# Kernel tuning notes

Measured on AMD Instinct MI355X. Metric: run time of the kernel, lower is better.

Reference implementation:

```python
import jax, jax.numpy as jnp
import numpy as np

H, D = 16, 64  # num_attention_heads, attention_head_size
BASE = 10000.0

def _rope(q, k, seq_len):
    # RotaryPositionalEmbedding: inv_freq over arange(0, D, 2); emb = cat(freqs, freqs)
    inv_freq = 1.0 / (BASE ** (jnp.arange(0, D, 2, dtype=jnp.float32) / D))  # [D/2]=32
    pos = jnp.arange(seq_len, dtype=jnp.float32)
    freqs = jnp.outer(pos, inv_freq)            # [S, 32]; equals cos_emb[..., :d]
    cos, sin = jnp.cos(freqs), jnp.sin(freqs)   # [S, 32]
    d = D // 2                                   # 32: only first half of head dim rotated
    half = d // 2                                # 16: internal rotate-half within rot part
    def rot(x):  # x: [B, H, S, D]
        xr, xp = x[..., :d], x[..., d:]
        swapped = jnp.concatenate([xr[..., half:], xr[..., :half]], axis=-1)
        xr2 = xr * cos - swapped * sin
        return jnp.concatenate([xr2, xp], axis=-1)
    return rot(q), rot(k)

def setup_inputs() -> dict:
    key = jax.random.key(0)
    ks = jax.random.split(key, 9)
    B, S, E = 2, 2048, 1024
    std = 0.02  # initializer_range
    inp = {"hidden_states": jax.random.normal(ks[0], (B, S, E), jnp.float32)}
    for i, n in enumerate(["q", "k", "v", "d"]):
        inp[f"W{n}"] = jax.random.normal(ks[1 + 2 * i], (E, E), jnp.float32) * std
        inp[f"b{n}"] = jnp.zeros((E,), jnp.float32)
    return inp

def reference(hidden_states, Wq, bq, Wk, bk, Wv, bv, Wd, bd):
    B, S, E = hidden_states.shape
    def heads(x):  # [B,S,E] -> [B,H,S,D]
        return x.reshape(B, S, H, D).transpose(0, 2, 1, 3)
    q = heads(hidden_states @ Wq + bq)
    k = heads(hidden_states @ Wk + bk)
    v = heads(hidden_states @ Wv + bv)
    q, k = _rope(q, k, S)
    scores = jnp.einsum("bhqd,bhkd->bhqk", q, k) / jnp.sqrt(jnp.float32(D))
    causal = jnp.tril(jnp.ones((S, S), dtype=bool))
    scores = jnp.where(causal, scores, -jnp.inf)
    probs = jax.nn.softmax(scores, axis=-1)
    ctx = jnp.einsum("bhqk,bhkd->bhqd", probs, v)
    ctx = ctx.transpose(0, 2, 1, 3).reshape(B, S, E)
    return ctx @ Wd + bd
```

## Files before the change

kernel.cpp:

```cpp
#include <hip/hip_runtime.h>
#include <stdint.h>

typedef __bf16 bf8 __attribute__((ext_vector_type(8)));
typedef float f4 __attribute__((ext_vector_type(4)));
typedef float f16v __attribute__((ext_vector_type(16)));
typedef unsigned short us8 __attribute__((ext_vector_type(8)));
typedef unsigned short us4 __attribute__((ext_vector_type(4)));

#define MFMA16(a, b, c) __builtin_amdgcn_mfma_f32_16x16x32_bf16(a, b, c, 0, 0, 0)
#define MFMA32(a, b, c) __builtin_amdgcn_mfma_f32_32x32x16_bf16(a, b, c, 0, 0, 0)

__device__ __forceinline__ unsigned short f2b(float f) {
  union { float f; unsigned u; } x; x.f = f;
  unsigned u = x.u;
  u += 0x7fffu + ((u >> 16) & 1u);
  return (unsigned short)(u >> 16);
}

__device__ __forceinline__ unsigned pk2(float a, float b) {
  union { float f; unsigned u; } ua, ub; ua.f = a; ub.f = b;
  return __builtin_amdgcn_perm(ub.u + 0x8000u, ua.u + 0x8000u, 0x07060302u);
}

__device__ __forceinline__ void plswap(unsigned &a, unsigned &b) {
  asm("v_permlane32_swap_b32 %0, %1" : "+v"(a), "+v"(b));
}

__device__ __forceinline__ void gload16(const void* g, void* l) {
  __builtin_amdgcn_global_load_lds(
      (const __attribute__((address_space(1))) void*)g,
      (__attribute__((address_space(3))) void*)l, 16, 0, 0);
}

__global__ __launch_bounds__(256) void prep_kernel(
    const float* __restrict__ W0, const float* __restrict__ W1,
    const float* __restrict__ W2, const float* __restrict__ W3,
    unsigned short* __restrict__ T0, unsigned short* __restrict__ T1,
    unsigned short* __restrict__ T2, unsigned short* __restrict__ T3,
    const float* __restrict__ hid, unsigned short* __restrict__ hb) {
  if (blockIdx.z == 4) {
    int bi = blockIdx.x + 32 * blockIdx.y;
#pragma unroll
    for (int k = 0; k < 4; ++k) {
      int i = bi * 1024 + k * 256 + threadIdx.x;
      float4 v = ((const float4*)hid)[i];
      us4 r = { f2b(v.x), f2b(v.y), f2b(v.z), f2b(v.w) };
      *(us4*)(hb + (size_t)i * 4) = r;
    }
    return;
  }
  const float* W; unsigned short* Wt;
  if (blockIdx.z == 0)      { W = W0; Wt = T0; }
  else if (blockIdx.z == 1) { W = W1; Wt = T1; }
  else if (blockIdx.z == 2) { W = W2; Wt = T2; }
  else                      { W = W3; Wt = T3; }
  __shared__ float tile[32][33];
  int tx = threadIdx.x & 31, ty = threadIdx.x >> 5;
  int kb = blockIdx.x * 32, nb = blockIdx.y * 32;
#pragma unroll
  for (int j = 0; j < 32; j += 8)
    tile[ty + j][tx] = W[(size_t)(kb + ty + j) * 1024 + nb + tx];
  __syncthreads();
#pragma unroll
  for (int j = 0; j < 32; j += 8)
    Wt[(size_t)(nb + ty + j) * 1024 + kb + tx] = f2b(tile[tx][ty + j]);
}

__global__ __launch_bounds__(256) void gemm_qkv_kernel(
    const unsigned short* __restrict__ X,
    const unsigned short* __restrict__ Wqt, const unsigned short* __restrict__ Wkt,
    const unsigned short* __restrict__ Wvt,
    const float* __restrict__ bq, const float* __restrict__ bk,
    const float* __restrict__ bv,
    unsigned short* __restrict__ Qo, unsigned short* __restrict__ Ko,
    unsigned short* __restrict__ Vo) {
  const unsigned short* Wt; const float* bias; unsigned short* out;
  if (blockIdx.z == 0)      { Wt = Wqt; bias = bq; out = Qo; }
  else if (blockIdx.z == 1) { Wt = Wkt; bias = bk; out = Ko; }
  else                      { Wt = Wvt; bias = bv; out = Vo; }

  __shared__ unsigned short As[128 * 32];
  __shared__ unsigned short Bs[128 * 32];
  const int t = threadIdx.x;
  const int wave = t >> 6, lane = t & 63, quad = lane >> 4, l16 = lane & 15;
  const int wm = (wave >> 1) * 64, wn = (wave & 1) * 64;
  const int m0 = blockIdx.y * 128, n0 = blockIdx.x * 128;

  f4 acc[4][4];
#pragma unroll
  for (int mi = 0; mi < 4; ++mi)
#pragma unroll
    for (int ni = 0; ni < 4; ++ni) acc[mi][ni] = (f4)0.0f;

  for (int k0 = 0; k0 < 1024; k0 += 32) {
    __syncthreads();
#pragma unroll
    for (int it = 0; it < 2; ++it) {
      int chunk = it * 256 + wave * 64 + lane;
      int row = chunk >> 2, c = chunk & 3;
      gload16(&X[(size_t)(m0 + row) * 1024 + k0 + c * 8],
              &As[(size_t)(it * 256 + wave * 64) * 8]);
      gload16(&Wt[(size_t)(n0 + row) * 1024 + k0 + c * 8],
              &Bs[(size_t)(it * 256 + wave * 64) * 8]);
    }
    __syncthreads();
    bf8 a[4], b[4];
#pragma unroll
    for (int mi = 0; mi < 4; ++mi)
      a[mi] = *(const bf8*)&As[(wm + mi * 16 + l16) * 32 + quad * 8];
#pragma unroll
    for (int ni = 0; ni < 4; ++ni)
      b[ni] = *(const bf8*)&Bs[(wn + ni * 16 + l16) * 32 + quad * 8];
#pragma unroll
    for (int mi = 0; mi < 4; ++mi)
#pragma unroll
      for (int ni = 0; ni < 4; ++ni)
        acc[mi][ni] = MFMA16(a[mi], b[ni], acc[mi][ni]);
  }

  float biasv[4];
#pragma unroll
  for (int ni = 0; ni < 4; ++ni) biasv[ni] = bias[n0 + wn + ni * 16 + l16];

  if (blockIdx.z < 2) {
    const float kr = 13.287712379549449f / 32.0f;
    const float f0 = exp2f(-(float)l16 * kr);
    const float f1 = exp2f(-(float)(l16 + 16) * kr);
    const float qs = (blockIdx.z == 0) ? 0.18033688011112042f : 1.0f;
#pragma unroll
    for (int mi = 0; mi < 4; ++mi) {
#pragma unroll
      for (int r = 0; r < 4; ++r) {
        int m = m0 + wm + mi * 16 + quad * 4 + r;
        float s = (float)(m & 2047);
        float s0, c0, s1, c1;
        __sincosf(s * f0, &s0, &c0);
        __sincosf(s * f1, &s1, &c1);
        float v0 = acc[mi][0][r] + biasv[0];
        float v1 = acc[mi][1][r] + biasv[1];
        acc[mi][0][r] = (v0 * c0 - v1 * s0) * qs;
        acc[mi][1][r] = (v1 * c1 - v0 * s1) * qs;
        acc[mi][2][r] = (acc[mi][2][r] + biasv[2]) * qs;
        acc[mi][3][r] = (acc[mi][3][r] + biasv[3]) * qs;
      }
    }
#pragma unroll
    for (int ni = 0; ni < 4; ++ni) {
      int n = n0 + wn + ni * 16 + l16;
      int h = n >> 6, d = n & 63;
#pragma unroll
      for (int mi = 0; mi < 4; ++mi) {
#pragma unroll
        for (int r = 0; r < 4; ++r) {
          int m = m0 + wm + mi * 16 + quad * 4 + r;
          int b_ = m >> 11, s = m & 2047;
          out[(size_t)(((b_ << 4) | h) * 2048 + s) * 64 + d] = f2b(acc[mi][ni][r]);
        }
      }
    }
  } else {
#pragma unroll
    for (int ni = 0; ni < 4; ++ni) {
      int n = n0 + wn + ni * 16 + l16;
      int h = n >> 6, d = n & 63;
#pragma unroll
      for (int mi = 0; mi < 4; ++mi) {
        int m = m0 + wm + mi * 16 + quad * 4;
        int b_ = m >> 11, s = m & 2047;
        us4 w = { f2b(acc[mi][ni][0] + biasv[ni]), f2b(acc[mi][ni][1] + biasv[ni]),
                  f2b(acc[mi][ni][2] + biasv[ni]), f2b(acc[mi][ni][3] + biasv[ni]) };
        *(us4*)&out[((size_t)(((b_ << 4) | h) * 64 + d)) * 2048 + s] = w;
      }
    }
  }
}

__global__ __launch_bounds__(256) void flash_attn_kernel(
    const unsigned short* __restrict__ Q, const unsigned short* __restrict__ K,
    const unsigned short* __restrict__ Vt, unsigned short* __restrict__ ctx) {
  __shared__ __align__(16) float osh[2][64][36];
  __shared__ float lsh[2][64];
  const int t = threadIdx.x;
  const int lane = t & 63;
  const int wave = t >> 6, l32 = lane & 31, hl = lane >> 5;
  const int sub = wave >> 1;
  const int kh  = wave & 1;

  const int id = blockIdx.x;
  const int bh = id & 31;
  const int j = id >> 5;
  const int qt = (j & 16) ? (31 - (j & 15)) : (j & 15);
  const int b = bh >> 4, h = bh & 15;

  const unsigned short* Qh = Q + (size_t)bh * 2048 * 64;
  const unsigned short* Kh = K + (size_t)bh * 2048 * 64;
  const unsigned short* Vh = Vt + (size_t)bh * 64 * 2048;

  const int wrow0 = qt * 64 + sub * 32;
  const int q = wrow0 + l32;

  bf8 qb[4];
#pragma unroll
  for (int c = 0; c < 4; ++c)
    qb[c] = *(const bf8*)&Qh[(size_t)q * 64 + c * 16 + hl * 8];

  f16v o0 = (f16v)0.0f, o1 = (f16v)0.0f;
  float sum = 0.0f;

  bf8 kfA[2][4], kfB[2][4], vf[2][4];
  const int nk = qt + 1;
  const int kb = kh ? (nk >> 1) : 0;
  const int ke = kh ? nk : (nk >> 1);

  auto loadK = [&](bf8 (&kf)[2][4], int k0) {
#pragma unroll
    for (int mt = 0; mt < 2; ++mt)
#pragma unroll
      for (int c = 0; c < 4; ++c)
        kf[mt][c] = *(const bf8*)&Kh[(size_t)(k0 + mt * 32 + l32) * 64 + c * 16 + hl * 8];
  };

  auto step = [&](int kt, bf8 (&kf)[2][4]) {
    const int k0 = kt * 64;
#pragma unroll
    for (int dt = 0; dt < 2; ++dt)
#pragma unroll
      for (int c = 0; c < 4; ++c)
        vf[dt][c] = *(const bf8*)&Vh[(size_t)(dt * 32 + l32) * 2048 + k0 + c * 16 + hl * 8];

    f16v s0 = (f16v)0.0f, s1 = (f16v)0.0f;
#pragma unroll
    for (int c = 0; c < 4; ++c) {
      s0 = MFMA32(kf[0][c], qb[c], s0);
      s1 = MFMA32(kf[1][c], qb[c], s1);
    }
    if (kt == nk - 1) {
#pragma unroll
      for (int gg = 0; gg < 4; ++gg)
#pragma unroll
        for (int i = 0; i < 4; ++i) {
          int kk = k0 + gg * 8 + hl * 4 + i;
          if (kk > q) s0[gg * 4 + i] = -3e38f;
          if (kk + 32 > q) s1[gg * 4 + i] = -3e38f;
        }
    }
    uint2 pd2[8];
#pragma unroll
    for (int gg = 0; gg < 4; ++gg) {
      float p0 = exp2f(s0[gg * 4 + 0]), p1 = exp2f(s0[gg * 4 + 1]);
      float p2 = exp2f(s0[gg * 4 + 2]), p3 = exp2f(s0[gg * 4 + 3]);
      sum += (p0 + p1) + (p2 + p3);
      pd2[gg].x = pk2(p0, p1); pd2[gg].y = pk2(p2, p3);
      float r0 = exp2f(s1[gg * 4 + 0]), r1 = exp2f(s1[gg * 4 + 1]);
      float r2 = exp2f(s1[gg * 4 + 2]), r3 = exp2f(s1[gg * 4 + 3]);
      sum += (r0 + r1) + (r2 + r3);
      pd2[4 + gg].x = pk2(r0, r1); pd2[4 + gg].y = pk2(r2, r3);
    }
    uint4 fr[4];
#pragma unroll
    for (int c = 0; c < 4; ++c) {
      unsigned ax = pd2[2 * c].x, bx = pd2[2 * c + 1].x;
      unsigned ay = pd2[2 * c].y, by = pd2[2 * c + 1].y;
      plswap(ax, bx);
      plswap(ay, by);
      fr[c].x = ax; fr[c].y = ay; fr[c].z = bx; fr[c].w = by;
    }
#pragma unroll
    for (int c = 0; c < 4; ++c) {
      union { uint4 u; bf8 v; } pv; pv.u = fr[c];
      o0 = MFMA32(vf[0][c], pv.v, o0);
      o1 = MFMA32(vf[1][c], pv.v, o1);
    }
  };

  if (kb < ke) {
    loadK(kfA, kb * 64);
    int kt = kb;
    while (true) {
      if (kt + 1 < ke) loadK(kfB, (kt + 1) * 64);
      step(kt, kfA);
      ++kt; if (kt >= ke) break;
      if (kt + 1 < ke) loadK(kfA, (kt + 1) * 64);
      step(kt, kfB);
      ++kt; if (kt >= ke) break;
    }
  }

  float lpart = sum + __shfl_xor(sum, 32);

  if (kh == 0) {
#pragma unroll
    for (int gg = 0; gg < 4; ++gg) {
      f4 w0 = { o0[gg * 4 + 0], o0[gg * 4 + 1], o0[gg * 4 + 2], o0[gg * 4 + 3] };
      *(f4*)&osh[sub][lane][gg * 4] = w0;
      f4 w1 = { o1[gg * 4 + 0], o1[gg * 4 + 1], o1[gg * 4 + 2], o1[gg * 4 + 3] };
      *(f4*)&osh[sub][lane][16 + gg * 4] = w1;
    }
    lsh[sub][lane] = lpart;
  }
  __syncthreads();
  if (kh == 1) {
    float inv = 1.0f / (lpart + lsh[sub][lane]);
#pragma unroll
    for (int gg = 0; gg < 4; ++gg) {
      int d0 = gg * 8 + hl * 4;
      f4 a0 = *(f4*)&osh[sub][lane][gg * 4];
      f4 a1 = *(f4*)&osh[sub][lane][16 + gg * 4];
      us4 w0 = { f2b((o0[gg * 4 + 0] + a0[0]) * inv), f2b((o0[gg * 4 + 1] + a0[1]) * inv),
                 f2b((o0[gg * 4 + 2] + a0[2]) * inv), f2b((o0[gg * 4 + 3] + a0[3]) * inv) };
      *(us4*)&ctx[((size_t)(b * 2048 + q)) * 1024 + h * 64 + d0] = w0;
      us4 w1 = { f2b((o1[gg * 4 + 0] + a1[0]) * inv), f2b((o1[gg * 4 + 1] + a1[1]) * inv),
                 f2b((o1[gg * 4 + 2] + a1[2]) * inv), f2b((o1[gg * 4 + 3] + a1[3]) * inv) };
      *(us4*)&ctx[((size_t)(b * 2048 + q)) * 1024 + h * 64 + 32 + d0] = w1;
    }
  }
}

__global__ __launch_bounds__(256) void gemm_out_kernel(
    const unsigned short* __restrict__ A,
    const unsigned short* __restrict__ Wt,
    const float* __restrict__ bias, float* __restrict__ out) {
  __shared__ unsigned short As[64 * 32];
  __shared__ unsigned short Bs[128 * 32];
  const int t = threadIdx.x;
  const int wave = t >> 6, lane = t & 63, quad = lane >> 4, l16 = lane & 15;
  const int wm = (wave & 1) * 32, wn = (wave >> 1) * 64;
  const int m0 = blockIdx.y * 64, n0 = blockIdx.x * 128;

  f4 acc[2][4];
#pragma unroll
  for (int mi = 0; mi < 2; ++mi)
#pragma unroll
    for (int ni = 0; ni < 4; ++ni) acc[mi][ni] = (f4)0.0f;

  for (int k0 = 0; k0 < 1024; k0 += 32) {
    __syncthreads();
    {
      int chunk = wave * 64 + lane;
      int row = chunk >> 2, c = chunk & 3;
      gload16(&A[(size_t)(m0 + row) * 1024 + k0 + c * 8],
              &As[(size_t)(wave * 64) * 8]);
#pragma unroll
      for (int it = 0; it < 2; ++it) {
        int ch = it * 256 + wave * 64 + lane;
        int rw = ch >> 2, cc = ch & 3;
        gload16(&Wt[(size_t)(n0 + rw) * 1024 + k0 + cc * 8],
                &Bs[(size_t)(it * 256 + wave * 64) * 8]);
      }
    }
    __syncthreads();
    bf8 a[2], b[4];
#pragma unroll
    for (int mi = 0; mi < 2; ++mi)
      a[mi] = *(const bf8*)&As[(wm + mi * 16 + l16) * 32 + quad * 8];
#pragma unroll
    for (int ni = 0; ni < 4; ++ni)
      b[ni] = *(const bf8*)&Bs[(wn + ni * 16 + l16) * 32 + quad * 8];
#pragma unroll
    for (int mi = 0; mi < 2; ++mi)
#pragma unroll
      for (int ni = 0; ni < 4; ++ni)
        acc[mi][ni] = MFMA16(a[mi], b[ni], acc[mi][ni]);
  }
#pragma unroll
  for (int ni = 0; ni < 4; ++ni) {
    int n = n0 + wn + ni * 16 + l16;
    float bv_ = bias[n];
#pragma unroll
    for (int mi = 0; mi < 2; ++mi) {
#pragma unroll
      for (int r = 0; r < 4; ++r) {
        int m = m0 + wm + mi * 16 + quad * 4 + r;
        out[(size_t)m * 1024 + n] = acc[mi][ni][r] + bv_;
      }
    }
  }
}

extern "C" void kernel_launch(void* const* d_in, const int* in_sizes, int n_in,
                              void* d_out, int out_size, void* d_ws, size_t ws_size,
                              hipStream_t stream) {
  const float* hidden = (const float*)d_in[0];
  const float* Wq = (const float*)d_in[1];
  const float* bq = (const float*)d_in[2];
  const float* Wk = (const float*)d_in[3];
  const float* bk = (const float*)d_in[4];
  const float* Wv = (const float*)d_in[5];
  const float* bv = (const float*)d_in[6];
  const float* Wd = (const float*)d_in[7];
  const float* bd = (const float*)d_in[8];
  float* out = (float*)d_out;

  char* ws = (char*)d_ws;
  unsigned short* Xb  = (unsigned short*)(ws);
  unsigned short* Wqt = (unsigned short*)(ws + ( 8ull << 20));
  unsigned short* Wkt = (unsigned short*)(ws + (10ull << 20));
  unsigned short* Wvt = (unsigned short*)(ws + (12ull << 20));
  unsigned short* Wdt = (unsigned short*)(ws + (14ull << 20));
  unsigned short* Qb  = (unsigned short*)(ws + (16ull << 20));
  unsigned short* Kb  = (unsigned short*)(ws + (24ull << 20));
  unsigned short* Vb  = (unsigned short*)(ws + (32ull << 20));
  unsigned short* Cb  = (unsigned short*)(ws + (40ull << 20));

  prep_kernel<<<dim3(32, 32, 5), 256, 0, stream>>>(
      Wq, Wk, Wv, Wd, Wqt, Wkt, Wvt, Wdt, hidden, Xb);
  gemm_qkv_kernel<<<dim3(8, 32, 3), 256, 0, stream>>>(
      Xb, Wqt, Wkt, Wvt, bq, bk, bv, Qb, Kb, Vb);
  flash_attn_kernel<<<1024, 256, 0, stream>>>(Qb, Kb, Vb, Cb);
  gemm_out_kernel<<<dim3(8, 64), 256, 0, stream>>>(Cb, Wdt, bd, out);
}
```

Before: 227.3 us.

## Store K and V in MFMA-fragment-tiled layout so attention loads are contiguous

The QKV projection epilogue now writes K and transposed V into a pre-swizzled layout that matches each lane's MFMA operand fragment for a 64-key tile. The flash attention kernel then loads each fragment as a fully contiguous per-lane 16-byte read (lane*8 offset) instead of strided row accesses. This is meant to improve coalescing and cut address arithmetic in the inner attention loop. The cost is scattered 2-byte stores for K in the projection epilogue, and the new layout couples the two kernels tightly.

```diff
diff --git a/kernel.cpp b/kernel.cpp
--- a/kernel.cpp
+++ b/kernel.cpp
@@ -144,32 +144,56 @@
         acc[mi][3][r] = (acc[mi][3][r] + biasv[3]) * qs;
       }
     }
+    if (blockIdx.z == 0) {
+#pragma unroll
+      for (int ni = 0; ni < 4; ++ni) {
+        int n = n0 + wn + ni * 16 + l16;
+        int h = n >> 6, d = n & 63;
+#pragma unroll
+        for (int mi = 0; mi < 4; ++mi) {
+#pragma unroll
+          for (int r = 0; r < 4; ++r) {
+            int m = m0 + wm + mi * 16 + quad * 4 + r;
+            int b_ = m >> 11, s = m & 2047;
+            out[(size_t)(((b_ << 4) | h) * 2048 + s) * 64 + d] = f2b(acc[mi][ni][r]);
+          }
+        }
+      }
+    } else {
+#pragma unroll
+      for (int ni = 0; ni < 4; ++ni) {
+        int n = n0 + wn + ni * 16 + l16;
+        int h = n >> 6, d = n & 63;
+        int cpart = (d >> 4) * 512 + ((d >> 3) & 1) * 256 + (d & 7);
+#pragma unroll
+        for (int mi = 0; mi < 4; ++mi) {
+#pragma unroll
+          for (int r = 0; r < 4; ++r) {
+            int m = m0 + wm + mi * 16 + quad * 4 + r;
+            int b_ = m >> 11, s = m & 2047;
+            size_t off = (size_t)((b_ << 4) | h) * 131072
+                       + (size_t)(s >> 5) * 2048 + (s & 31) * 8 + cpart;
+            out[off] = f2b(acc[mi][ni][r]);
+          }
+        }
+      }
+    }
+  } else {
 #pragma unroll
     for (int ni = 0; ni < 4; ++ni) {
       int n = n0 + wn + ni * 16 + l16;
       int h = n >> 6, d = n & 63;
-#pragma unroll
-      for (int mi = 0; mi < 4; ++mi) {
-#pragma unroll
-        for (int r = 0; r < 4; ++r) {
-          int m = m0 + wm + mi * 16 + quad * 4 + r;
-          int b_ = m >> 11, s = m & 2047;
-          out[(size_t)(((b_ << 4) | h) * 2048 + s) * 64 + d] = f2b(acc[mi][ni][r]);
-        }
-      }
-    }
-  } else {
-#pragma unroll
-    for (int ni = 0; ni < 4; ++ni) {
-      int n = n0 + wn + ni * 16 + l16;
-      int h = n >> 6, d = n & 63;
+      int dpart = ((d >> 5) & 1) * 2048 + (d & 31) * 8;
 #pragma unroll
       for (int mi = 0; mi < 4; ++mi) {
         int m = m0 + wm + mi * 16 + quad * 4;
         int b_ = m >> 11, s = m & 2047;
         us4 w = { f2b(acc[mi][ni][0] + biasv[ni]), f2b(acc[mi][ni][1] + biasv[ni]),
                   f2b(acc[mi][ni][2] + biasv[ni]), f2b(acc[mi][ni][3] + biasv[ni]) };
-        *(us4*)&out[((size_t)(((b_ << 4) | h) * 64 + d)) * 2048 + s] = w;
+        size_t off = (size_t)((b_ << 4) | h) * 131072
+                   + (size_t)(s >> 6) * 4096 + ((s >> 4) & 3) * 512
+                   + ((s >> 3) & 1) * 256 + dpart + (s & 7);
+        *(us4*)&out[off] = w;
       }
     }
   }
@@ -192,9 +216,9 @@
   const int qt = (j & 16) ? (31 - (j & 15)) : (j & 15);
   const int b = bh >> 4, h = bh & 15;
 
-  const unsigned short* Qh = Q + (size_t)bh * 2048 * 64;
-  const unsigned short* Kh = K + (size_t)bh * 2048 * 64;
-  const unsigned short* Vh = Vt + (size_t)bh * 64 * 2048;
+  const unsigned short* Qh = Q + (size_t)bh * 131072;
+  const unsigned short* Kh = K + (size_t)bh * 131072;
+  const unsigned short* Vh = Vt + (size_t)bh * 131072;
 
   const int wrow0 = qt * 64 + sub * 32;
   const int q = wrow0 + l32;
@@ -212,21 +236,23 @@
   const int kb = kh ? (nk >> 1) : 0;
   const int ke = kh ? nk : (nk >> 1);
 
-  auto loadK = [&](bf8 (&kf)[2][4], int k0) {
+  auto loadK = [&](bf8 (&kf)[2][4], int kt) {
+    const unsigned short* p = Kh + (size_t)kt * 4096 + lane * 8;
 #pragma unroll
     for (int mt = 0; mt < 2; ++mt)
 #pragma unroll
       for (int c = 0; c < 4; ++c)
-        kf[mt][c] = *(const bf8*)&Kh[(size_t)(k0 + mt * 32 + l32) * 64 + c * 16 + hl * 8];
+        kf[mt][c] = *(const bf8*)&p[mt * 2048 + c * 512];
   };
 
   auto step = [&](int kt, bf8 (&kf)[2][4]) {
     const int k0 = kt * 64;
+    const unsigned short* pv = Vh + (size_t)kt * 4096 + lane * 8;
 #pragma unroll
     for (int dt = 0; dt < 2; ++dt)
 #pragma unroll
       for (int c = 0; c < 4; ++c)
-        vf[dt][c] = *(const bf8*)&Vh[(size_t)(dt * 32 + l32) * 2048 + k0 + c * 16 + hl * 8];
+        vf[dt][c] = *(const bf8*)&pv[dt * 2048 + c * 512];
 
     f16v s0 = (f16v)0.0f, s1 = (f16v)0.0f;
 #pragma unroll
@@ -267,20 +293,20 @@
     }
 #pragma unroll
     for (int c = 0; c < 4; ++c) {
-      union { uint4 u; bf8 v; } pv; pv.u = fr[c];
-      o0 = MFMA32(vf[0][c], pv.v, o0);
-      o1 = MFMA32(vf[1][c], pv.v, o1);
+      union { uint4 u; bf8 v; } pv2; pv2.u = fr[c];
+      o0 = MFMA32(vf[0][c], pv2.v, o0);
+      o1 = MFMA32(vf[1][c], pv2.v, o1);
     }
   };
 
   if (kb < ke) {
-    loadK(kfA, kb * 64);
+    loadK(kfA, kb);
     int kt = kb;
     while (true) {
-      if (kt + 1 < ke) loadK(kfB, (kt + 1) * 64);
+      if (kt + 1 < ke) loadK(kfB, kt + 1);
       step(kt, kfA);
       ++kt; if (kt >= ke) break;
-      if (kt + 1 < ke) loadK(kfA, (kt + 1) * 64);
+      if (kt + 1 < ke) loadK(kfA, kt + 1);
       step(kt, kfB);
       ++kt; if (kt >= ke) break;
     }
```

After: 205.3 us. -9.7%, faster.
